# Kernel tuning notes

Measured on AMD Instinct MI355X. Metric: run time of the kernel, lower is better.

Reference implementation:

```python
import jax, jax.numpy as jnp
import numpy as np

GRID_DIM = 7
NQUERIES = 100
C = 256

def setup_inputs() -> dict:
    key = jax.random.key(0)
    k1, k2 = jax.random.split(key)
    images = jax.random.normal(k1, (4, 224, 224, C), dtype=jnp.float32)
    # learned query weight (orthogonal init in original; random normal is fine as a stand-in)
    queries = jax.random.normal(k2, (NQUERIES, C), dtype=jnp.float32)
    return {"images": images, "queries": queries}

def _positions(g):
    lin = jnp.linspace(0.0, 1.0, g + 1)[:-1].astype(jnp.float32)
    # positions[i*g + j] = (lin[i], lin[j]) -> (h_frac, w_frac), row-major over the grid
    return jnp.stack(jnp.meshgrid(lin, lin, indexing="ij"), axis=-1).reshape(g * g, 2)

def reference(images, queries):
    g = GRID_DIM
    B, H, W, Cc = images.shape
    h, w = H // g, W // g
    # batch-extract all grid regions at once: [B, g*g, h*w, C]
    regions = images.reshape(B, g, h, g, w, Cc)
    regions = regions.transpose(0, 1, 3, 2, 4, 5).reshape(B, g * g, h * w, Cc)
    # keras Attention (dot, no scale): softmax(Q K^T) V, queries shared across batch/regions
    scores = jnp.einsum("qc,bnsc->bnqs", queries, regions)  # [B, g*g, nq, h*w]
    attn = jax.nn.softmax(scores, axis=-1)
    out = jnp.einsum("bnqs,bnsc->bnqc", attn, regions)  # [B, g*g, nq, C]
    return out, _positions(g)
```

## Files before the change

### kernel.cpp

```cpp
#include <hip/hip_runtime.h>
#include <stdint.h>

typedef short short8 __attribute__((ext_vector_type(8)));
typedef __fp16 fp16x8 __attribute__((ext_vector_type(8)));
typedef float f32x16 __attribute__((ext_vector_type(16)));
typedef unsigned int uint;

#define NREG 49
#define NQ   100
#define CC   256
#define OUT_POS_OFF 5017600
#define PO_PER (NQ*CC)
#define QF_BYTES 65536
#define MFMA_BF16 __builtin_amdgcn_mfma_f32_32x32x16_bf16
#define MFMA_F16  __builtin_amdgcn_mfma_f32_32x32x16_f16

union U4H8 { uint4 u; fp16x8 h; short8 s; };

#define LBAR() do { \
    asm volatile("s_waitcnt lgkmcnt(0)" ::: "memory"); \
    __builtin_amdgcn_s_barrier(); \
} while (0)

__device__ __forceinline__ uint pkrtz(float a, float b){
    auto v = __builtin_amdgcn_cvt_pkrtz(a, b);
    return __builtin_bit_cast(uint, v);
}
__device__ __forceinline__ uint16_t f2bf_rne(float x){
    uint u = __float_as_uint(x);
    u += 0x7fffu + ((u >> 16) & 1u);
    return (uint16_t)(u >> 16);
}
__device__ __forceinline__ float bf2f(uint16_t b){
    return __uint_as_float(((uint)b) << 16);
}

__global__ __launch_bounds__(512) void qfrag_kernel(const float* __restrict__ Qg,
                                                    uint4* __restrict__ qf){
    int gid  = blockIdx.x * 512 + threadIdx.x;
    int lane = gid & 63;
    int frag = gid >> 6;
    int k    = frag & 15;
    int qt   = frag >> 4;
    int q    = qt * 32 + (lane & 31);
    int c0   = k * 16 + (lane >> 5) * 8;
    float v[8];
#pragma unroll
    for (int j = 0; j < 8; ++j) v[j] = (q < NQ) ? Qg[q * CC + c0 + j] : 0.f;
    qf[gid] = make_uint4(pkrtz(v[0], v[1]), pkrtz(v[2], v[3]),
                         pkrtz(v[4], v[5]), pkrtz(v[6], v[7]));
}

__global__ __launch_bounds__(512, 2) void attn_kernel(
        const float* __restrict__ img, const uint4* __restrict__ qf,
        float* __restrict__ out, float* __restrict__ po,
        float* __restrict__ pl, int split)
{
    __shared__ __align__(16) unsigned char smem[65536];
    unsigned char* sRT = smem;
    unsigned char* sU  = smem + 32768;

    const int tid = threadIdx.x;
    const int seg = blockIdx.x % split;
    const int bn  = blockIdx.x / split;
    const int rr  = bn % NREG;
    const int bb  = bn / NREG;
    const int gh  = rr / 7, gw = rr % 7;

    if (bn == 0 && seg == 0 && tid < NREG){
        out[OUT_POS_OFF + 2 * tid]     = (float)((tid / 7) / 7.0);
        out[OUT_POS_OFF + 2 * tid + 1] = (float)((tid % 7) / 7.0);
    }

    const int lane = tid & 63, w = tid >> 6;
    const int l31  = lane & 31;
    const int st = w & 1, qt = w >> 1;
    const int mp = w & 1, cq = w >> 1;

    const int kA    = lane >> 2;
    const int aInP  = 32 * ((lane >> 1) & 1) * 16 + (lane & 1) * 8;
    const int aSwz  = (kA & 7) << 4;
    const int cb    = lane >> 3;
    const int c31b  = 4 * (lane & 7);

    const float* rbase = img + ((size_t)(bb * 224 + gh * 32) * 224 + gw * 32) * CC;

    uint4 qr[16];
#pragma unroll
    for (int k = 0; k < 16; ++k) qr[k] = qf[(qt * 16 + k) * 64 + lane];

    f32x16 acc00, acc01, acc10, acc11;
#pragma unroll
    for (int i = 0; i < 16; ++i){ acc00[i]=0.f; acc01[i]=0.f; acc10[i]=0.f; acc11[i]=0.f; }
    float lp = 0.f;
    const int qq = qt * 32 + l31;

    const int nch = 16 / split;
    const int ch0 = seg * nch, ch1 = ch0 + nch;

    float4 rb[8], rb2[8];
    {
#pragma unroll
        for (int j = 0; j < 8; ++j){
            int p = ch0 * 64 + j * 8 + w;
            rb[j] = *(const float4*)(rbase + ((p >> 5) * 224 + (p & 31)) * CC + 4 * lane);
        }
    }

    for (int ch = ch0; ch < ch1; ++ch){
#pragma unroll
        for (int j = 0; j < 8; ++j){
            int pl_ = j * 8 + w;
            int frag  = (pl_ >> 5) * 16 + kA;
            int inner = (((pl_ & 31) * 16 + aInP)) ^ aSwz;
            uint2 val = make_uint2(pkrtz(rb[j].x, rb[j].y), pkrtz(rb[j].z, rb[j].w));
            *(uint2*)(sU + frag * 1024 + inner) = val;
            const float* fv = (const float*)&rb[j];
            int fbase = ((j >> 1) * 8 + cb) * 1024 + (j & 1) * 512 + w * 2;
#pragma unroll
            for (int cc = 0; cc < 4; ++cc){
                uint u = __float_as_uint(fv[cc]);
                *(uint16_t*)(sRT + fbase + (((c31b + cc) ^ cb) << 4)) = (uint16_t)(u >> 16);
            }
        }

        if (ch + 1 < ch1){
#pragma unroll
            for (int j = 0; j < 8; ++j){
                int p = (ch + 1) * 64 + j * 8 + w;
                rb2[j] = *(const float4*)(rbase + ((p >> 5) * 224 + (p & 31)) * CC + 4 * lane);
            }
        }
        LBAR();

        f32x16 a1;
#pragma unroll
        for (int i = 0; i < 16; ++i) a1[i] = 0.f;
#pragma unroll
        for (int k = 0; k < 16; ++k){
            U4H8 af; af.u = *(const uint4*)(sU + (st * 16 + k) * 1024 + ((lane * 16) ^ ((k & 7) << 4)));
            U4H8 bq; bq.u = qr[k];
            a1 = MFMA_F16(af.h, bq.h, a1, 0, 0, 0);
        }
        LBAR();

#pragma unroll
        for (int g2 = 0; g2 < 4; ++g2){
            uint16_t e[4];
#pragma unroll
            for (int r2 = 0; r2 < 4; ++r2){
                float sc = a1[g2 * 4 + r2];
                float pv = exp2f(sc * 1.4426950408889634f - 57.70780163555852f);
                e[r2] = f2bf_rne(pv);
                lp += bf2f(e[r2]);
            }
            int kst = st * 2 + (g2 >> 1);
            int boff = ((kst * 4 + qt) * 64 + (g2 & 1) * 32 + l31) * 16 + (lane >> 5) * 8;
            *(uint2*)(sU + boff) = make_uint2((uint)e[0] | ((uint)e[1] << 16),
                                              (uint)e[2] | ((uint)e[3] << 16));
        }
        LBAR();

#pragma unroll
        for (int ks = 0; ks < 4; ++ks){
            U4H8 A0, A1, B0, B1;
            A0.u = *(const uint4*)(sU  + ((ks * 4 + mp * 2    ) * 64 + lane) * 16);
            A1.u = *(const uint4*)(sU  + ((ks * 4 + mp * 2 + 1) * 64 + lane) * 16);
            B0.u = *(const uint4*)(sRT + ((ks * 8 + cq * 2    ) * 64 + (lane ^ (cq * 2    ))) * 16);
            B1.u = *(const uint4*)(sRT + ((ks * 8 + cq * 2 + 1) * 64 + (lane ^ (cq * 2 + 1))) * 16);
            acc00 = MFMA_BF16(A0.s, B0.s, acc00, 0, 0, 0);
            acc01 = MFMA_BF16(A0.s, B1.s, acc01, 0, 0, 0);
            acc10 = MFMA_BF16(A1.s, B0.s, acc10, 0, 0, 0);
            acc11 = MFMA_BF16(A1.s, B1.s, acc11, 0, 0, 0);
        }
        LBAR();

        if (ch + 1 < ch1){
#pragma unroll
            for (int j = 0; j < 8; ++j) rb[j] = rb2[j];
        }
    }

    float* sL = (float*)sU;
    if (tid < 128) sL[tid] = 0.f;
    __syncthreads();
    atomicAdd(&sL[qq], lp);
    __syncthreads();

    const int c0 = cq * 64 + l31;
    if (split == 1){
        float* ob = out + (size_t)bn * PO_PER;
#pragma unroll
        for (int r = 0; r < 16; ++r){
            int row = (r & 3) + 8 * (r >> 2) + 4 * (lane >> 5);
            int q0 = mp * 64 + row, q1 = q0 + 32;
            if (q0 < NQ){
                float inv = 1.0f / sL[q0];
                ob[q0 * CC + c0]      = acc00[r] * inv;
                ob[q0 * CC + c0 + 32] = acc01[r] * inv;
            }
            if (q1 < NQ){
                float inv = 1.0f / sL[q1];
                ob[q1 * CC + c0]      = acc10[r] * inv;
                ob[q1 * CC + c0 + 32] = acc11[r] * inv;
            }
        }
    } else {
        float* ob = po + ((size_t)bn * split + seg) * PO_PER;
#pragma unroll
        for (int r = 0; r < 16; ++r){
            int row = (r & 3) + 8 * (r >> 2) + 4 * (lane >> 5);
            int q0 = mp * 64 + row, q1 = q0 + 32;
            if (q0 < NQ){
                ob[q0 * CC + c0]      = acc00[r];
                ob[q0 * CC + c0 + 32] = acc01[r];
            }
            if (q1 < NQ){
                ob[q1 * CC + c0]      = acc10[r];
                ob[q1 * CC + c0 + 32] = acc11[r];
            }
        }
        if (tid < 128) pl[((size_t)bn * split + seg) * 128 + tid] = sL[tid];
    }
}

__global__ __launch_bounds__(512) void reduce_kernel(
        const float* __restrict__ po, const float* __restrict__ pl,
        float* __restrict__ out, int split)
{
    __shared__ float sInv[64];
    const int bn = blockIdx.x >> 1, hf = blockIdx.x & 1, tid = threadIdx.x;
    if (tid < 50){
        int q = hf * 50 + tid;
        float s = 0.f;
        for (int g = 0; g < split; ++g)
            s += pl[((size_t)bn * split + g) * 128 + q];
        sInv[tid] = 1.0f / s;
    }
    __syncthreads();
    const float* base = po + (size_t)bn * split * PO_PER;
    float* ob = out + (size_t)bn * PO_PER;
#pragma unroll 1
    for (int i = 0; i < 25; ++i){
        int idx = hf * 12800 + i * 512 + tid;
        float s = 0.f;
        for (int g = 0; g < split; ++g) s += base[g * PO_PER + idx];
        ob[idx] = s * sInv[(idx >> 8) - hf * 50];
    }
}

extern "C" void kernel_launch(void* const* d_in, const int* in_sizes, int n_in,
                              void* d_out, int out_size, void* d_ws, size_t ws_size,
                              hipStream_t stream){
    const float* img = (const float*)d_in[0];
    const float* Qg  = (const float*)d_in[1];
    float* out = (float*)d_out;

    uint4* qf = (uint4*)d_ws;
    qfrag_kernel<<<8, 512, 0, stream>>>(Qg, qf);

    int split = 1;
    const size_t per_seg = (size_t)196 * (PO_PER + 128) * sizeof(float);
    if (ws_size >= QF_BYTES + 4 * per_seg) split = 4;

    float *po = nullptr, *pl = nullptr;
    if (split > 1){
        po = (float*)((char*)d_ws + QF_BYTES);
        pl = po + (size_t)196 * split * PO_PER;
    }

    attn_kernel<<<196 * split, 512, 0, stream>>>(img, qf, out, po, pl, split);
    if (split > 1)
        reduce_kernel<<<392, 512, 0, stream>>>(po, pl, out, split);
}
```

Measured before the change: 354.1 us.

## Use persistent stream-K style work split with per-slot partials and tagged reduction

Replaces the fixed split-by-4 grid (784 blocks) with 256 blocks. Each block takes a contiguous range of 12 or 13 chunk units that can cross a region boundary, and it flushes up to two partial results into tagged slots. The reduce kernel finds the slots for each region by scanning the tags and sums them. The aim is to balance work across the 256 CUs and remove tail waves, at the cost of extra syncs in the flush path and a tag scan in the reduce step. It also drops the split==1 fallback and assumes the workspace is large enough.

```diff
diff --git a/kernel.cpp b/kernel.cpp
--- a/kernel.cpp
+++ b/kernel.cpp
@@ -12,6 +12,8 @@
 #define OUT_POS_OFF 5017600
 #define PO_PER (NQ*CC)
 #define QF_BYTES 65536
+#define NBLK 256
+#define NSLOT (NBLK*2)
 #define MFMA_BF16 __builtin_amdgcn_mfma_f32_32x32x16_bf16
 #define MFMA_F16  __builtin_amdgcn_mfma_f32_32x32x16_f16
 
@@ -54,20 +56,16 @@
 __global__ __launch_bounds__(512, 2) void attn_kernel(
         const float* __restrict__ img, const uint4* __restrict__ qf,
         float* __restrict__ out, float* __restrict__ po,
-        float* __restrict__ pl, int split)
+        float* __restrict__ pl, int* __restrict__ tg)
 {
     __shared__ __align__(16) unsigned char smem[65536];
     unsigned char* sRT = smem;
     unsigned char* sU  = smem + 32768;
 
     const int tid = threadIdx.x;
-    const int seg = blockIdx.x % split;
-    const int bn  = blockIdx.x / split;
-    const int rr  = bn % NREG;
-    const int bb  = bn / NREG;
-    const int gh  = rr / 7, gw = rr % 7;
-
-    if (bn == 0 && seg == 0 && tid < NREG){
+    const int b   = blockIdx.x;
+
+    if (b == 0 && tid < NREG){
         out[OUT_POS_OFF + 2 * tid]     = (float)((tid / 7) / 7.0);
         out[OUT_POS_OFF + 2 * tid + 1] = (float)((tid % 7) / 7.0);
     }
@@ -76,6 +74,7 @@
     const int l31  = lane & 31;
     const int st = w & 1, qt = w >> 1;
     const int mp = w & 1, cq = w >> 1;
+    const int c0 = cq * 64 + l31;
 
     const int kA    = lane >> 2;
     const int aInP  = 32 * ((lane >> 1) & 1) * 16 + (lane & 1) * 8;
@@ -83,8 +82,6 @@
     const int cb    = lane >> 3;
     const int c31b  = 4 * (lane & 7);
 
-    const float* rbase = img + ((size_t)(bb * 224 + gh * 32) * 224 + gw * 32) * CC;
-
     uint4 qr[16];
 #pragma unroll
     for (int k = 0; k < 16; ++k) qr[k] = qf[(qt * 16 + k) * 64 + lane];
@@ -95,19 +92,67 @@
     float lp = 0.f;
     const int qq = qt * 32 + l31;
 
-    const int nch = 16 / split;
-    const int ch0 = seg * nch, ch1 = ch0 + nch;
+    const int cnt = 12 + (b < 64 ? 1 : 0);
+    const int u0  = b * 12 + (b < 64 ? b : 64);
+    const int u1  = u0 + cnt;
+
+    auto rebase = [&](int u) -> const float* {
+        int bn = u >> 4;
+        int rr = bn % NREG, bb = bn / NREG;
+        int gh = rr / 7,    gw = rr % 7;
+        return img + ((size_t)(bb * 224 + gh * 32) * 224 + gw * 32) * CC;
+    };
+
+    auto flush = [&](int bn_, int fi_){
+        __syncthreads();
+        float* sL = (float*)sU;
+        if (tid < 128) sL[tid] = 0.f;
+        __syncthreads();
+        atomicAdd(&sL[qq], lp);
+        __syncthreads();
+        const int slot = b * 2 + fi_;
+        float* ob = po + (size_t)slot * PO_PER;
+#pragma unroll
+        for (int r = 0; r < 16; ++r){
+            int row = (r & 3) + 8 * (r >> 2) + 4 * (lane >> 5);
+            int q0 = mp * 64 + row, q1 = q0 + 32;
+            if (q0 < NQ){
+                ob[q0 * CC + c0]      = acc00[r];
+                ob[q0 * CC + c0 + 32] = acc01[r];
+            }
+            if (q1 < NQ){
+                ob[q1 * CC + c0]      = acc10[r];
+                ob[q1 * CC + c0 + 32] = acc11[r];
+            }
+        }
+        if (tid < 128) pl[(size_t)slot * 128 + tid] = sL[tid];
+        if (tid == 0)  tg[slot] = bn_;
+        __syncthreads();
+    };
 
     float4 rb[8], rb2[8];
     {
+        const float* rbase = rebase(u0);
+        int ch = u0 & 15;
 #pragma unroll
         for (int j = 0; j < 8; ++j){
-            int p = ch0 * 64 + j * 8 + w;
+            int p = ch * 64 + j * 8 + w;
             rb[j] = *(const float4*)(rbase + ((p >> 5) * 224 + (p & 31)) * CC + 4 * lane);
         }
     }
 
-    for (int ch = ch0; ch < ch1; ++ch){
+    int cur_bn = u0 >> 4, fi = 0;
+
+    for (int u = u0; u < u1; ++u){
+        int bn = u >> 4;
+        if (bn != cur_bn){
+            flush(cur_bn, fi);
+            fi = 1; cur_bn = bn;
+#pragma unroll
+            for (int i = 0; i < 16; ++i){ acc00[i]=0.f; acc01[i]=0.f; acc10[i]=0.f; acc11[i]=0.f; }
+            lp = 0.f;
+        }
+
 #pragma unroll
         for (int j = 0; j < 8; ++j){
             int pl_ = j * 8 + w;
@@ -119,16 +164,18 @@
             int fbase = ((j >> 1) * 8 + cb) * 1024 + (j & 1) * 512 + w * 2;
 #pragma unroll
             for (int cc = 0; cc < 4; ++cc){
-                uint u = __float_as_uint(fv[cc]);
-                *(uint16_t*)(sRT + fbase + (((c31b + cc) ^ cb) << 4)) = (uint16_t)(u >> 16);
-            }
-        }
-
-        if (ch + 1 < ch1){
+                uint uu = __float_as_uint(fv[cc]);
+                *(uint16_t*)(sRT + fbase + (((c31b + cc) ^ cb) << 4)) = (uint16_t)(uu >> 16);
+            }
+        }
+
+        if (u + 1 < u1){
+            const float* rbase2 = rebase(u + 1);
+            int ch2 = (u + 1) & 15;
 #pragma unroll
             for (int j = 0; j < 8; ++j){
-                int p = (ch + 1) * 64 + j * 8 + w;
-                rb2[j] = *(const float4*)(rbase + ((p >> 5) * 224 + (p & 31)) * CC + 4 * lane);
+                int p = ch2 * 64 + j * 8 + w;
+                rb2[j] = *(const float4*)(rbase2 + ((p >> 5) * 224 + (p & 31)) * CC + 4 * lane);
             }
         }
         LBAR();
@@ -175,76 +222,50 @@
         }
         LBAR();
 
-        if (ch + 1 < ch1){
+        if (u + 1 < u1){
 #pragma unroll
             for (int j = 0; j < 8; ++j) rb[j] = rb2[j];
         }
     }
 
-    float* sL = (float*)sU;
-    if (tid < 128) sL[tid] = 0.f;
-    __syncthreads();
-    atomicAdd(&sL[qq], lp);
-    __syncthreads();
-
-    const int c0 = cq * 64 + l31;
-    if (split == 1){
-        float* ob = out + (size_t)bn * PO_PER;
-#pragma unroll
-        for (int r = 0; r < 16; ++r){
-            int row = (r & 3) + 8 * (r >> 2) + 4 * (lane >> 5);
-            int q0 = mp * 64 + row, q1 = q0 + 32;
-            if (q0 < NQ){
-                float inv = 1.0f / sL[q0];
-                ob[q0 * CC + c0]      = acc00[r] * inv;
-                ob[q0 * CC + c0 + 32] = acc01[r] * inv;
-            }
-            if (q1 < NQ){
-                float inv = 1.0f / sL[q1];
-                ob[q1 * CC + c0]      = acc10[r] * inv;
-                ob[q1 * CC + c0 + 32] = acc11[r] * inv;
-            }
-        }
-    } else {
-        float* ob = po + ((size_t)bn * split + seg) * PO_PER;
-#pragma unroll
-        for (int r = 0; r < 16; ++r){
-            int row = (r & 3) + 8 * (r >> 2) + 4 * (lane >> 5);
-            int q0 = mp * 64 + row, q1 = q0 + 32;
-            if (q0 < NQ){
-                ob[q0 * CC + c0]      = acc00[r];
-                ob[q0 * CC + c0 + 32] = acc01[r];
-            }
-            if (q1 < NQ){
-                ob[q1 * CC + c0]      = acc10[r];
-                ob[q1 * CC + c0 + 32] = acc11[r];
-            }
-        }
-        if (tid < 128) pl[((size_t)bn * split + seg) * 128 + tid] = sL[tid];
-    }
+    flush(cur_bn, fi);
+    if (fi == 0 && tid == 0) tg[b * 2 + 1] = -1;
 }
 
 __global__ __launch_bounds__(512) void reduce_kernel(
         const float* __restrict__ po, const float* __restrict__ pl,
-        float* __restrict__ out, int split)
+        const int* __restrict__ tg, float* __restrict__ out)
 {
+    __shared__ int slots[8];
+    __shared__ int ns;
     __shared__ float sInv[64];
     const int bn = blockIdx.x >> 1, hf = blockIdx.x & 1, tid = threadIdx.x;
+
+    if (tid == 0) ns = 0;
+    __syncthreads();
+    if (tid < NSLOT && tg[tid] == bn){
+        int i = atomicAdd(&ns, 1);
+        slots[i] = tid;
+    }
+    __syncthreads();
+    const int n = ns;
+
     if (tid < 50){
         int q = hf * 50 + tid;
         float s = 0.f;
-        for (int g = 0; g < split; ++g)
-            s += pl[((size_t)bn * split + g) * 128 + q];
+        for (int i = 0; i < n; ++i)
+            s += pl[(size_t)slots[i] * 128 + q];
         sInv[tid] = 1.0f / s;
     }
     __syncthreads();
-    const float* base = po + (size_t)bn * split * PO_PER;
+
     float* ob = out + (size_t)bn * PO_PER;
 #pragma unroll 1
     for (int i = 0; i < 25; ++i){
         int idx = hf * 12800 + i * 512 + tid;
         float s = 0.f;
-        for (int g = 0; g < split; ++g) s += base[g * PO_PER + idx];
+        for (int j = 0; j < n; ++j)
+            s += po[(size_t)slots[j] * PO_PER + idx];
         ob[idx] = s * sInv[(idx >> 8) - hf * 50];
     }
 }
@@ -257,19 +278,11 @@
     float* out = (float*)d_out;
 
     uint4* qf = (uint4*)d_ws;
+    float* po = (float*)((char*)d_ws + QF_BYTES);
+    float* pl = po + (size_t)NSLOT * PO_PER;
+    int*   tg = (int*)(pl + (size_t)NSLOT * 128);
+
     qfrag_kernel<<<8, 512, 0, stream>>>(Qg, qf);
-
-    int split = 1;
-    const size_t per_seg = (size_t)196 * (PO_PER + 128) * sizeof(float);
-    if (ws_size >= QF_BYTES + 4 * per_seg) split = 4;
-
-    float *po = nullptr, *pl = nullptr;
-    if (split > 1){
-        po = (float*)((char*)d_ws + QF_BYTES);
-        pl = po + (size_t)196 * split * PO_PER;
-    }
-
-    attn_kernel<<<196 * split, 512, 0, stream>>>(img, qf, out, po, pl, split);
-    if (split > 1)
-        reduce_kernel<<<392, 512, 0, stream>>>(po, pl, out, split);
-}
+    attn_kernel<<<NBLK, 512, 0, stream>>>(img, qf, out, po, pl, tg);
+    reduce_kernel<<<392, 512, 0, stream>>>(po, pl, tg, out);
+}
```

Measured after the change: 335.4 us. 5.3% less time.
